# Kernel optimization log

Measured on AMD Instinct MI355X. Metric: run time of the kernel, lower is better.

Reference implementation:

```python
import math
import jax, jax.numpy as jnp
import numpy as np

B, S, D, H = 8, 4096, 1024, 16
DH = D // H


def setup_inputs() -> dict:
    key = jax.random.key(0)
    ks = jax.random.split(key, 12)
    std = 0.02
    inp = {
        "hidden_states": jax.random.normal(ks[0], (B, S, D), jnp.float32),
        "attention_mask": jnp.zeros((B, 1, S), jnp.float32),
        # Linear params stored as (in, out); torch Linear computes x @ W.T + b,
        # equivalent to x @ W_here + b with W_here = W_torch.T
        "Wq": jax.random.normal(ks[1], (D, D), jnp.float32) * std,
        "bq": jnp.zeros((D,), jnp.float32),
        "Wqa": jax.random.normal(ks[2], (D, H), jnp.float32) * std,
        "bqa": jnp.zeros((H,), jnp.float32),
        "Wk": jax.random.normal(ks[3], (D, D), jnp.float32) * std,
        "bk": jnp.zeros((D,), jnp.float32),
        "Wka": jax.random.normal(ks[4], (D, H), jnp.float32) * std,
        "bka": jnp.zeros((H,), jnp.float32),
        "Wt": jax.random.normal(ks[5], (D, D), jnp.float32) * std,
        "bt": jnp.zeros((D,), jnp.float32),
    }
    return inp


def reference(hidden_states, attention_mask, Wq, bq, Wqa, bqa, Wk, bk, Wka, bka, Wt, bt):
    b, s, d = hidden_states.shape
    h = Wqa.shape[1]
    dh = d // h
    scale = 1.0 / math.sqrt(dh)

    q = hidden_states @ Wq + bq                      # (B,S,D)
    k = hidden_states @ Wk + bk                      # (B,S,D)

    # query pooling weights: (B,H,S)
    q_score = jnp.swapaxes((q @ Wqa + bqa) * scale, 1, 2) + attention_mask
    q_weight = jax.nn.softmax(q_score, axis=-1)

    q_heads = q.reshape(b, s, h, dh)                 # (B,S,H,dh)
    # pooled query per head -> flatten to (B,1,D); broadcast replaces repeat
    pooled_q = jnp.einsum('bhs,bshd->bhd', q_weight, q_heads).reshape(b, 1, d)

    mixed_qk = k * pooled_q                          # (B,S,D)

    # key pooling weights: (B,H,S)
    k_score = jnp.swapaxes((mixed_qk @ Wka + bka) * scale, 1, 2) + attention_mask
    k_weight = jax.nn.softmax(k_score, axis=-1)

    k_heads = mixed_qk.reshape(b, s, h, dh)
    pooled_k = jnp.einsum('bhs,bshd->bhd', k_weight, k_heads)   # (B,H,dh)

    weighted = (pooled_k[:, None, :, :] * q_heads).reshape(b, s, d)  # (B,S,D)
    return weighted @ Wt + bt + q
```

## Files before the change

kernel.cpp:

```cpp
#include <hip/hip_runtime.h>


typedef unsigned short u16;
typedef float f32x4 __attribute__((ext_vector_type(4)));
typedef short bf16x8 __attribute__((ext_vector_type(8)));

#define DEV __device__ __forceinline__

DEV u16 f2bf(float f) {
  union { float f; unsigned u; } c; c.f = f;
  return (u16)((c.u + 0x7FFFu + ((c.u >> 16) & 1u)) >> 16);
}
DEV float bf2f(u16 h) {
  union { unsigned u; float f; } c; c.u = ((unsigned)h) << 16;
  return c.f;
}

#define SBAR_ __builtin_amdgcn_s_barrier()

__global__ __launch_bounds__(256) void k_cvt(const float* __restrict__ in,
                                             u16* __restrict__ out, int n4) {
  int i = blockIdx.x * 256 + threadIdx.x;
  const int stride = gridDim.x * 256;
  for (; i < n4; i += stride) {
    float4 v = reinterpret_cast<const float4*>(in)[i];
    ushort4 o;
    o.x = f2bf(v.x); o.y = f2bf(v.y); o.z = f2bf(v.z); o.w = f2bf(v.w);
    reinterpret_cast<ushort4*>(out)[i] = o;
  }
}

__global__ __launch_bounds__(256) void k_transw(const float* __restrict__ Wq,
                                                const float* __restrict__ Wk,
                                                const float* __restrict__ Wt,
                                                u16* __restrict__ Wqkt,
                                                u16* __restrict__ Wtt) {
  __shared__ float tile[32][33];
  const int z = blockIdx.z;
  const float* W = (z == 0) ? Wq : (z == 1) ? Wk : Wt;
  u16* D = (z == 0) ? Wqkt : (z == 1) ? (Wqkt + 1024 * 1024) : Wtt;
  const int bn = blockIdx.x, bk = blockIdx.y;
  const int tx = threadIdx.x & 31, ty = threadIdx.x >> 5;
#pragma unroll
  for (int j = 0; j < 4; ++j)
    tile[ty + j * 8][tx] = W[(size_t)(bk * 32 + ty + j * 8) * 1024 + bn * 32 + tx];
  __syncthreads();
#pragma unroll
  for (int j = 0; j < 4; ++j)
    D[(size_t)(bn * 32 + ty + j * 8) * 1024 + bk * 32 + tx] = f2bf(tile[tx][ty + j * 8]);
}

__global__ __launch_bounds__(256) void k_wbt(const u16* __restrict__ Wtt,
                                             const float* __restrict__ pkr,
                                             const float* __restrict__ pqr,
                                             const float* __restrict__ sumk,
                                             const float* __restrict__ sumq,
                                             u16* __restrict__ Wbt) {
  const int i = blockIdx.x * 256 + threadIdx.x;
  const int k0 = (i & 127) * 8;
  const int n  = (i >> 7) & 1023;
  const int b  = i >> 17;
  const int hh = k0 >> 6;
  const float inv = 1.0f / (sumk[b * 16 + hh] * sumq[b * 16 + hh]);
  bf16x8 wv = *reinterpret_cast<const bf16x8*>(&Wtt[n * 1024 + k0]);
  bf16x8 o;
#pragma unroll
  for (int j = 0; j < 8; ++j) {
    const float p = pkr[b * 1024 + k0 + j] * pqr[b * 1024 + k0 + j] * inv;
    const float ident = (k0 + j == n) ? 1.0f : 0.0f;
    o[j] = (short)f2bf(bf2f((u16)wv[j]) * p + ident);
  }
  *reinterpret_cast<bf16x8*>(&Wbt[(size_t)b * 1048576 + (size_t)n * 1024 + k0]) = o;
}

template <int EPI>
__global__ __launch_bounds__(512, 2) void k_gemm8(const u16* __restrict__ A,
                                                  const u16* __restrict__ Bt,
                                                  const float* __restrict__ bias0,
                                                  const float* __restrict__ bias1,
                                                  float* __restrict__ Cf,
                                                  u16* __restrict__ C0,
                                                  u16* __restrict__ C1,
                                                  int gcols) {
  __shared__ __align__(16) u16 lds[2 * 32768];
  const int tid = threadIdx.x;
  const int w = tid >> 6, lane = tid & 63;
  const int wm = w >> 2, wn = w & 3;

  const int nwg = gridDim.x;
  const int swz = (blockIdx.x & 7) * (nwg >> 3) + (blockIdx.x >> 3);
  const int ci = swz % gcols, ri = swz / gcols;
  const int row0 = ri * 256, col0 = ci * 256;

  const int sr = tid >> 3;
  const int ls8 = ((tid & 7) ^ (sr & 7)) * 8;
  const u16* gA = A + (size_t)(row0 + sr) * 1024 + ls8;
  const u16* gB;
  if (EPI == 2) {
    gB = Bt + (size_t)(row0 >> 12) * 1048576 + (size_t)(col0 + sr) * 1024 + ls8;
  } else {
    gB = Bt + (size_t)(col0 + sr) * 1024 + ls8;
  }

  auto stage = [&](int buf, int mat, int half, int kt, const u16* g) {
#pragma unroll
    for (int p = 0; p < 2; ++p) {
      const u16* src = g + (size_t)(half * 128 + p * 64) * 1024 + kt;
      u16* dst = (u16*)&lds[buf * 32768 + mat * 16384 + half * 8192 + p * 4096 + w * 512];
      __builtin_amdgcn_global_load_lds(
          (const __attribute__((address_space(1))) void*)src,
          (__attribute__((address_space(3))) void*)dst, 16, 0, 0);
    }
  };

  f32x4 acc[8][4] = {};

  stage(0, 0, 0, 0, gA);
  stage(0, 0, 1, 0, gA);
  stage(0, 1, 0, 0, gB);
  stage(0, 1, 1, 0, gB);
  stage(1, 1, 0, 64, gB);
  stage(1, 1, 1, 64, gB);
  asm volatile("s_waitcnt vmcnt(4)" ::: "memory");
  SBAR_;

  const int lr15 = lane & 15, lhi = lane >> 4, lx = lane & 7;
  bf16x8 A0f[4][2], A1f[4][2], B0f[2][2], B1f[2][2];

#define RD_Ah(dst, base, half)                                                 \
  _Pragma("unroll") for (int mi = 0; mi < 4; ++mi)                             \
  _Pragma("unroll") for (int ks = 0; ks < 2; ++ks)                             \
    dst[mi][ks] = *reinterpret_cast<const bf16x8*>(                            \
        &(base)[(wm * 128 + (half) * 64 + mi * 16 + lr15) * 64 +               \
                (((ks << 2) | lhi) ^ lx) * 8]);
#define RD_Bh(dst, base, half)                                                 \
  _Pragma("unroll") for (int ni = 0; ni < 2; ++ni)                             \
  _Pragma("unroll") for (int ks = 0; ks < 2; ++ks)                             \
    dst[ni][ks] = *reinterpret_cast<const bf16x8*>(                            \
        &(base)[(wn * 64 + (half) * 32 + ni * 16 + lr15) * 64 +                \
                (((ks << 2) | lhi) ^ lx) * 8]);
#define MFMA_Q(ar, br, mo, no)                                                 \
  _Pragma("unroll") for (int mi = 0; mi < 4; ++mi)                             \
  _Pragma("unroll") for (int ni = 0; ni < 2; ++ni)                             \
  _Pragma("unroll") for (int ks = 0; ks < 2; ++ks)                             \
    acc[(mo) + mi][(no) + ni] = __builtin_amdgcn_mfma_f32_16x16x32_bf16(       \
        ar[mi][ks], br[ni][ks], acc[(mo) + mi][(no) + ni], 0, 0, 0);

#define LGKM0_ asm volatile("s_waitcnt lgkmcnt(0)" ::: "memory")
#define LGKM8_ asm volatile("s_waitcnt lgkmcnt(8)" ::: "memory")
#define PRIO1_ __builtin_amdgcn_s_setprio(1)
#define PRIO0_ __builtin_amdgcn_s_setprio(0)

  const u16* bA0 = &lds[0];
  const u16* bB0 = bA0 + 16384;
  const u16* bA1 = &lds[32768];
  const u16* bB1 = bA1 + 16384;

  for (int i = 0; i < 8; ++i) {
    const int t1k = (2 * i + 1) * 64;
    const int t2k = (2 * i + 2) * 64;
    const int t3k = (2 * i + 3) * 64;
    const bool pf = (i < 7);

    RD_Ah(A0f, bA0, 0);
    RD_Bh(B0f, bB0, 0);
    stage(1, 0, 0, t1k, gA);
    LGKM8_;
    SBAR_;
    LGKM0_;
    PRIO1_; MFMA_Q(A0f, B0f, 0, 0); PRIO0_;
    SBAR_;

    RD_Bh(B1f, bB0, 1);
    stage(1, 0, 1, t1k, gA);
    SBAR_;
    LGKM0_;
    PRIO1_; MFMA_Q(A0f, B1f, 0, 2); PRIO0_;
    SBAR_;

    RD_Ah(A1f, bA0, 1);
    if (pf) stage(0, 1, 0, t2k, gB);
    SBAR_;
    LGKM0_;
    PRIO1_; MFMA_Q(A1f, B1f, 4, 2); PRIO0_;
    SBAR_;

    if (pf) {
      stage(0, 1, 1, t2k, gB);
      asm volatile("s_waitcnt vmcnt(4)" ::: "memory");
    } else {
      asm volatile("s_waitcnt vmcnt(0)" ::: "memory");
    }
    SBAR_;
    PRIO1_; MFMA_Q(A1f, B0f, 4, 0); PRIO0_;
    SBAR_;

    RD_Ah(A0f, bA1, 0);
    RD_Bh(B0f, bB1, 0);
    if (pf) stage(0, 0, 0, t2k, gA);
    LGKM8_;
    SBAR_;
    LGKM0_;
    PRIO1_; MFMA_Q(A0f, B0f, 0, 0); PRIO0_;
    SBAR_;

    RD_Bh(B1f, bB1, 1);
    if (pf) stage(0, 0, 1, t2k, gA);
    SBAR_;
    LGKM0_;
    PRIO1_; MFMA_Q(A0f, B1f, 0, 2); PRIO0_;
    SBAR_;

    RD_Ah(A1f, bA1, 1);
    if (pf) stage(1, 1, 0, t3k, gB);
    SBAR_;
    LGKM0_;
    PRIO1_; MFMA_Q(A1f, B1f, 4, 2); PRIO0_;
    SBAR_;

    if (pf) {
      stage(1, 1, 1, t3k, gB);
      asm volatile("s_waitcnt vmcnt(4)" ::: "memory");
    }
    SBAR_;
    PRIO1_; MFMA_Q(A1f, B0f, 4, 0); PRIO0_;
    SBAR_;
  }
#undef RD_Ah
#undef RD_Bh
#undef MFMA_Q
#undef LGKM0_
#undef LGKM8_
#undef PRIO1_
#undef PRIO0_

  if constexpr (EPI == 0) {
    u16* cl = (u16*)lds;
    const bool lo = (ci < (gcols >> 1));
    const float* bias = lo ? bias0 : bias1;
    u16* dst = lo ? C0 : C1;
    const int colloc0 = col0 - (lo ? 0 : 1024);
#pragma unroll
    for (int n = 0; n < 4; ++n) {
      const int cc = wn * 64 + n * 16 + lr15;
      const float bv = bias[colloc0 + cc];
#pragma unroll
      for (int m = 0; m < 8; ++m) {
        const int rb = wm * 128 + m * 16 + lhi * 4;
#pragma unroll
        for (int j = 0; j < 4; ++j) {
          const int r = rb + j;
          cl[r * 256 + (cc ^ ((r & 12) << 2))] = f2bf(acc[m][n][j] + bv);
        }
      }
    }
    __syncthreads();
#pragma unroll
    for (int pass = 0; pass < 16; ++pass) {
      const int idx = pass * 512 + tid;
      const int r = idx >> 5, g = idx & 31;
      bf16x8 v = *reinterpret_cast<const bf16x8*>(
          &cl[r * 256 + ((g * 8) ^ ((r & 12) << 2))]);
      *reinterpret_cast<bf16x8*>(
          &dst[(size_t)(row0 + r) * 1024 + colloc0 + g * 8]) = v;
    }
  } else {
    float* clf = (float*)lds;
#pragma unroll
    for (int half = 0; half < 2; ++half) {
      __syncthreads();
      if (wm == half) {
#pragma unroll
        for (int n = 0; n < 4; ++n) {
          const int cc = wn * 64 + n * 16 + lr15;
#pragma unroll
          for (int m = 0; m < 8; ++m) {
            const int rb = m * 16 + lhi * 4;
#pragma unroll
            for (int j = 0; j < 4; ++j) {
              const int r = rb + j;
              clf[r * 256 + (cc ^ ((r & 12) << 2))] = acc[m][n][j];
            }
          }
        }
      }
      __syncthreads();
#pragma unroll
      for (int pass = 0; pass < 16; ++pass) {
        const int idx = pass * 512 + tid;
        const int r = idx >> 6, g = idx & 63;
        f32x4 v = *reinterpret_cast<const f32x4*>(
            &clf[r * 256 + ((g * 4) ^ ((r & 12) << 2))]);
        const int grow = row0 + half * 128 + r;
        const int gcol = col0 + g * 4;
        float4 o;
        o.x = v[0] + bias0[gcol + 0];
        o.y = v[1] + bias0[gcol + 1];
        o.z = v[2] + bias0[gcol + 2];
        o.w = v[3] + bias0[gcol + 3];
        *reinterpret_cast<float4*>(&Cf[(size_t)grow * 1024 + gcol]) = o;
      }
    }
  }
}

template <int HAS_PQ>
__global__ __launch_bounds__(256, 2) void k_scoreg(const u16* __restrict__ X,
                                                   const float* __restrict__ Wa,
                                                   const float* __restrict__ bias,
                                                   const float* __restrict__ mask,
                                                   const float* __restrict__ pqr,
                                                   const float* __restrict__ sumq,
                                                   float* __restrict__ wexp,
                                                   float* __restrict__ sumexp,
                                                   float scale) {
  __shared__ __align__(16) u16 bw[16 * 1024];
  __shared__ __align__(16) u16 lA[2 * 128 * 64];
  __shared__ float invs[16];
  const int tid = threadIdx.x;
  const int w = tid >> 6, lane = tid & 63;
  const int row0 = blockIdx.x * 128;
  const int b = row0 >> 12;
  const int si0 = row0 & 4095;

  if (HAS_PQ) {
    if (tid < 16) invs[tid] = 1.0f / sumq[b * 16 + tid];
    __syncthreads();
  }
  for (int t = tid; t < 16384; t += 256) {
    const int k = t >> 4, h = t & 15;
    float wv = Wa[t];
    if (HAS_PQ) wv *= pqr[b * 1024 + k] * invs[k >> 6];
    bw[h * 1024 + (k ^ ((h & 7) << 3))] = f2bf(wv);
  }

  const int sr = tid >> 3;
  const int ls8 = ((tid & 7) ^ (sr & 7)) * 8;
  const u16* gA = X + (size_t)(row0 + sr) * 1024 + ls8;
  auto stage = [&](int buf, int kt) {
#pragma unroll
    for (int p = 0; p < 4; ++p) {
      const u16* src = gA + (size_t)(p * 32) * 1024 + kt;
      u16* dst = &lA[buf * 8192 + p * 2048 + tid * 8];
      __builtin_amdgcn_global_load_lds(
          (const __attribute__((address_space(1))) void*)src,
          (__attribute__((address_space(3))) void*)dst, 16, 0, 0);
    }
  };

  f32x4 acc[2] = {};
  stage(0, 0);
  stage(1, 64);
  asm volatile("s_waitcnt vmcnt(4) lgkmcnt(0)" ::: "memory");
  SBAR_;

  const int lr15 = lane & 15, lhi = lane >> 4, lx = lane & 7;
  bf16x8 Af[2][2], Bf[2];

  int cur = 0;
  for (int t = 0; t < 16; ++t) {
    const u16* bA = &lA[cur * 8192];
    const int kt = t * 64;
#pragma unroll
    for (int mi = 0; mi < 2; ++mi)
#pragma unroll
      for (int ks = 0; ks < 2; ++ks)
        Af[mi][ks] = *reinterpret_cast<const bf16x8*>(
            &bA[(w * 32 + mi * 16 + lr15) * 64 + (((ks << 2) | lhi) ^ lx) * 8]);
#pragma unroll
    for (int ks = 0; ks < 2; ++ks)
      Bf[ks] = *reinterpret_cast<const bf16x8*>(
          &bw[lr15 * 1024 + ((kt + ks * 32 + lhi * 8) ^ ((lr15 & 7) << 3))]);
#pragma unroll
    for (int mi = 0; mi < 2; ++mi)
#pragma unroll
      for (int ks = 0; ks < 2; ++ks)
        acc[mi] = __builtin_amdgcn_mfma_f32_16x16x32_bf16(
            Af[mi][ks], Bf[ks], acc[mi], 0, 0, 0);
    SBAR_;
    if (t < 14) {
      stage(cur, (t + 2) * 64);
      asm volatile("s_waitcnt vmcnt(4)" ::: "memory");
    } else if (t == 14) {
      asm volatile("s_waitcnt vmcnt(0)" ::: "memory");
    }
    SBAR_;
    cur ^= 1;
  }
  SBAR_;

  float* wl = (float*)lA;
#pragma unroll
  for (int mi = 0; mi < 2; ++mi)
#pragma unroll
    for (int j = 0; j < 4; ++j) {
      const int row = w * 32 + mi * 16 + lhi * 4 + j;
      const float v = (acc[mi][j] + bias[lr15]) * scale +
                      mask[b * 4096 + si0 + row];
      wl[lr15 * 132 + row] = __expf(v);
    }
  __syncthreads();
  {
    const int h = tid >> 4, part = tid & 15;
    float s = 0.f;
#pragma unroll
    for (int j = 0; j < 8; ++j) s += wl[h * 132 + part * 8 + j];
#pragma unroll
    for (int m = 1; m < 16; m <<= 1) s += __shfl_xor(s, m, 64);
    if (part == 0) atomicAdd(&sumexp[b * 16 + h], s);
  }
  if (tid < 128) {
    const int h = tid >> 3, g = tid & 7;
#pragma unroll
    for (int q4 = 0; q4 < 4; ++q4) {
      f32x4 v = *reinterpret_cast<const f32x4*>(&wl[h * 132 + g * 16 + q4 * 4]);
      *reinterpret_cast<f32x4*>(
          &wexp[((size_t)b * 16 + h) * 4096 + si0 + g * 16 + q4 * 4]) = v;
    }
  }
}

__global__ __launch_bounds__(256) void k_pool(const float* __restrict__ wexp,
                                              const u16* __restrict__ X,
                                              float* __restrict__ pooled) {
  __shared__ float wl[16][132];
  const int b = blockIdx.x >> 5, c = blockIdx.x & 31;
  const int s0 = c * 128;
  for (int t = threadIdx.x; t < 2048; t += 256) {
    const int h = t >> 7, si = t & 127;
    wl[h][si] = wexp[((size_t)b * 16 + h) * 4096 + s0 + si];
  }
  __syncthreads();
  const int d0 = threadIdx.x * 4, h = threadIdx.x >> 4;
  float a0 = 0, a1 = 0, a2 = 0, a3 = 0;
#pragma unroll 4
  for (int si = 0; si < 128; ++si) {
    const float wv = wl[h][si];
    const size_t base = ((size_t)b * 4096 + s0 + si) * 1024 + d0;
    ushort4 xq = *reinterpret_cast<const ushort4*>(X + base);
    a0 += wv * bf2f(xq.x); a1 += wv * bf2f(xq.y);
    a2 += wv * bf2f(xq.z); a3 += wv * bf2f(xq.w);
  }
  atomicAdd(&pooled[b * 1024 + d0 + 0], a0);
  atomicAdd(&pooled[b * 1024 + d0 + 1], a1);
  atomicAdd(&pooled[b * 1024 + d0 + 2], a2);
  atomicAdd(&pooled[b * 1024 + d0 + 3], a3);
}

extern "C" void kernel_launch(void* const* d_in, const int* in_sizes, int n_in,
                              void* d_out, int out_size, void* d_ws, size_t ws_size,
                              hipStream_t stream) {
  (void)in_sizes; (void)n_in; (void)out_size; (void)ws_size;
  const float* x    = (const float*)d_in[0];
  const float* mask = (const float*)d_in[1];
  const float* Wq   = (const float*)d_in[2];
  const float* bq   = (const float*)d_in[3];
  const float* Wqa  = (const float*)d_in[4];
  const float* bqa  = (const float*)d_in[5];
  const float* Wk   = (const float*)d_in[6];
  const float* bk   = (const float*)d_in[7];
  const float* Wka  = (const float*)d_in[8];
  const float* bka  = (const float*)d_in[9];
  const float* Wt   = (const float*)d_in[10];
  const float* bt   = (const float*)d_in[11];
  float* out = (float*)d_out;
  char* ws = (char*)d_ws;

  size_t off = 0;
  auto take = [&](size_t b) { char* p = ws + off; off += (b + 255) & ~(size_t)255; return p; };
  u16*   xb    = (u16*)  take(67108864);
  u16*   qb    = (u16*)  take(67108864);
  u16*   kb    = (u16*)  take(67108864);
  u16*   Wqkt  = (u16*)  take(4194304);
  u16*   Wtt   = (u16*)  take(2097152);
  u16*   Wbt   = (u16*)  take(16777216);
  float* wexp  = (float*)take(2097152);
  char*  nb    = take(68608);
  float* pqr  = (float*)nb;
  float* pkr  = (float*)(nb + 32768);
  float* sumq = (float*)(nb + 65536);
  float* sumk = (float*)(nb + 66048);

  k_cvt<<<2048, 256, 0, stream>>>(x, xb, 8388608);
  k_transw<<<dim3(32, 32, 3), 256, 0, stream>>>(Wq, Wk, Wt, Wqkt, Wtt);
  hipMemsetAsync(nb, 0, 68608, stream);

  k_gemm8<0><<<1024, 512, 0, stream>>>(xb, Wqkt, bq, bk, nullptr, qb, kb, 8);

  k_scoreg<0><<<256, 256, 0, stream>>>(qb, Wqa, bqa, mask, nullptr, nullptr,
                                       wexp, sumq, 0.125f);
  k_pool<<<256, 256, 0, stream>>>(wexp, qb, pqr);

  k_scoreg<1><<<256, 256, 0, stream>>>(kb, Wka, bka, mask, pqr, sumq,
                                       wexp, sumk, 0.125f);
  k_pool<<<256, 256, 0, stream>>>(wexp, kb, pkr);

  k_wbt<<<4096, 256, 0, stream>>>(Wtt, pkr, pqr, sumk, sumq, Wbt);
  k_gemm8<2><<<512, 512, 0, stream>>>(qb, Wbt, bt, nullptr, out, nullptr, nullptr, 4);
}
```

Baseline: 362.1 us.

## Fold key projection into pooling algebra to drop the K GEMM

The full K projection GEMM and the bf16 K buffer are removed. The key score weights are folded into combined per-batch matrices, (Wk·diag(pooled_q))·Wka plus bias, so scores come straight from x. Pooled q and pooled k are computed by pooling x per head and then multiplying by the transposed weights in a small kernel. This halves the large first GEMM and cuts intermediate traffic. In exchange it adds a naive weight-combine kernel, 16 MB partial-sum buffers and an extra reduction pass per pooling stage.

```diff
diff --git a/kernel.cpp b/kernel.cpp
--- a/kernel.cpp
+++ b/kernel.cpp
@@ -33,12 +33,13 @@
 __global__ __launch_bounds__(256) void k_transw(const float* __restrict__ Wq,
                                                 const float* __restrict__ Wk,
                                                 const float* __restrict__ Wt,
-                                                u16* __restrict__ Wqkt,
+                                                u16* __restrict__ Wqt,
+                                                u16* __restrict__ Wkt,
                                                 u16* __restrict__ Wtt) {
   __shared__ float tile[32][33];
   const int z = blockIdx.z;
   const float* W = (z == 0) ? Wq : (z == 1) ? Wk : Wt;
-  u16* D = (z == 0) ? Wqkt : (z == 1) ? (Wqkt + 1024 * 1024) : Wtt;
+  u16* D = (z == 0) ? Wqt : (z == 1) ? Wkt : Wtt;
   const int bn = blockIdx.x, bk = blockIdx.y;
   const int tx = threadIdx.x & 31, ty = threadIdx.x >> 5;
 #pragma unroll
@@ -50,23 +51,49 @@
     D[(size_t)(bn * 32 + ty + j * 8) * 1024 + bk * 32 + tx] = f2bf(tile[tx][ty + j * 8]);
 }
 
+template <int WEIGHTED>
+__global__ __launch_bounds__(256) void k_wcmb(const float* __restrict__ Wsrc,
+                                              const float* __restrict__ Wa,
+                                              const float* __restrict__ bsrc,
+                                              const float* __restrict__ ba,
+                                              const float* __restrict__ pqn,
+                                              float* __restrict__ Wc,
+                                              float* __restrict__ bc) {
+  const int b = blockIdx.y;
+  const int e = blockIdx.x * 16 + (threadIdx.x >> 4);
+  const int h = threadIdx.x & 15;
+  float s = 0.f;
+  for (int d = 0; d < 1024; ++d) {
+    float w = Wsrc[(size_t)e * 1024 + d] * Wa[d * 16 + h];
+    if (WEIGHTED) w *= pqn[b * 1024 + d];
+    s += w;
+  }
+  Wc[((size_t)b * 1024 + e) * 16 + h] = s;
+  if (blockIdx.x == 0 && threadIdx.x < 16) {
+    const int hh = threadIdx.x;
+    float sb = ba[hh];
+    for (int d = 0; d < 1024; ++d) {
+      float w = bsrc[d] * Wa[d * 16 + hh];
+      if (WEIGHTED) w *= pqn[b * 1024 + d];
+      sb += w;
+    }
+    bc[b * 16 + hh] = sb;
+  }
+}
+
 __global__ __launch_bounds__(256) void k_wbt(const u16* __restrict__ Wtt,
-                                             const float* __restrict__ pkr,
-                                             const float* __restrict__ pqr,
-                                             const float* __restrict__ sumk,
-                                             const float* __restrict__ sumq,
+                                             const float* __restrict__ pqn,
+                                             const float* __restrict__ pkn,
                                              u16* __restrict__ Wbt) {
   const int i = blockIdx.x * 256 + threadIdx.x;
   const int k0 = (i & 127) * 8;
   const int n  = (i >> 7) & 1023;
   const int b  = i >> 17;
-  const int hh = k0 >> 6;
-  const float inv = 1.0f / (sumk[b * 16 + hh] * sumq[b * 16 + hh]);
   bf16x8 wv = *reinterpret_cast<const bf16x8*>(&Wtt[n * 1024 + k0]);
   bf16x8 o;
 #pragma unroll
   for (int j = 0; j < 8; ++j) {
-    const float p = pkr[b * 1024 + k0 + j] * pqr[b * 1024 + k0 + j] * inv;
+    const float p = pqn[b * 1024 + k0 + j] * pkn[b * 1024 + k0 + j];
     const float ident = (k0 + j == n) ? 1.0f : 0.0f;
     o[j] = (short)f2bf(bf2f((u16)wv[j]) * p + ident);
   }
@@ -77,10 +104,8 @@
 __global__ __launch_bounds__(512, 2) void k_gemm8(const u16* __restrict__ A,
                                                   const u16* __restrict__ Bt,
                                                   const float* __restrict__ bias0,
-                                                  const float* __restrict__ bias1,
                                                   float* __restrict__ Cf,
                                                   u16* __restrict__ C0,
-                                                  u16* __restrict__ C1,
                                                   int gcols) {
   __shared__ __align__(16) u16 lds[2 * 32768];
   const int tid = threadIdx.x;
@@ -236,14 +261,10 @@
 
   if constexpr (EPI == 0) {
     u16* cl = (u16*)lds;
-    const bool lo = (ci < (gcols >> 1));
-    const float* bias = lo ? bias0 : bias1;
-    u16* dst = lo ? C0 : C1;
-    const int colloc0 = col0 - (lo ? 0 : 1024);
 #pragma unroll
     for (int n = 0; n < 4; ++n) {
       const int cc = wn * 64 + n * 16 + lr15;
-      const float bv = bias[colloc0 + cc];
+      const float bv = bias0[col0 + cc];
 #pragma unroll
       for (int m = 0; m < 8; ++m) {
         const int rb = wm * 128 + m * 16 + lhi * 4;
@@ -262,7 +283,7 @@
       bf16x8 v = *reinterpret_cast<const bf16x8*>(
           &cl[r * 256 + ((g * 8) ^ ((r & 12) << 2))]);
       *reinterpret_cast<bf16x8*>(
-          &dst[(size_t)(row0 + r) * 1024 + colloc0 + g * 8]) = v;
+          &C0[(size_t)(row0 + r) * 1024 + col0 + g * 8]) = v;
     }
   } else {
     float* clf = (float*)lds;
@@ -304,34 +325,27 @@
   }
 }
 
-template <int HAS_PQ>
 __global__ __launch_bounds__(256, 2) void k_scoreg(const u16* __restrict__ X,
-                                                   const float* __restrict__ Wa,
+                                                   const float* __restrict__ Weff,
                                                    const float* __restrict__ bias,
                                                    const float* __restrict__ mask,
-                                                   const float* __restrict__ pqr,
-                                                   const float* __restrict__ sumq,
                                                    float* __restrict__ wexp,
                                                    float* __restrict__ sumexp,
-                                                   float scale) {
+                                                   float scale, int wstride,
+                                                   int bstride) {
   __shared__ __align__(16) u16 bw[16 * 1024];
   __shared__ __align__(16) u16 lA[2 * 128 * 64];
-  __shared__ float invs[16];
   const int tid = threadIdx.x;
   const int w = tid >> 6, lane = tid & 63;
   const int row0 = blockIdx.x * 128;
   const int b = row0 >> 12;
   const int si0 = row0 & 4095;
 
-  if (HAS_PQ) {
-    if (tid < 16) invs[tid] = 1.0f / sumq[b * 16 + tid];
-    __syncthreads();
-  }
+  const float* Wb = Weff + (size_t)b * wstride;
+  const float* bb = bias + b * bstride;
   for (int t = tid; t < 16384; t += 256) {
     const int k = t >> 4, h = t & 15;
-    float wv = Wa[t];
-    if (HAS_PQ) wv *= pqr[b * 1024 + k] * invs[k >> 6];
-    bw[h * 1024 + (k ^ ((h & 7) << 3))] = f2bf(wv);
+    bw[h * 1024 + (k ^ ((h & 7) << 3))] = f2bf(Wb[t]);
   }
 
   const int sr = tid >> 3;
@@ -395,7 +409,7 @@
 #pragma unroll
     for (int j = 0; j < 4; ++j) {
       const int row = w * 32 + mi * 16 + lhi * 4 + j;
-      const float v = (acc[mi][j] + bias[lr15]) * scale +
+      const float v = (acc[mi][j] + bb[lr15]) * scale +
                       mask[b * 4096 + si0 + row];
       wl[lr15 * 132 + row] = __expf(v);
     }
@@ -420,9 +434,9 @@
   }
 }
 
-__global__ __launch_bounds__(256) void k_pool(const float* __restrict__ wexp,
-                                              const u16* __restrict__ X,
-                                              float* __restrict__ pooled) {
+__global__ __launch_bounds__(256) void k_poolx(const float* __restrict__ wexp,
+                                               const u16* __restrict__ X,
+                                               float* __restrict__ PXpart) {
   __shared__ float wl[16][132];
   const int b = blockIdx.x >> 5, c = blockIdx.x & 31;
   const int s0 = c * 128;
@@ -431,20 +445,59 @@
     wl[h][si] = wexp[((size_t)b * 16 + h) * 4096 + s0 + si];
   }
   __syncthreads();
-  const int d0 = threadIdx.x * 4, h = threadIdx.x >> 4;
+  const int e0 = threadIdx.x * 4;
+  float acc[16][4] = {};
+#pragma unroll 2
+  for (int si = 0; si < 128; ++si) {
+    const size_t base = ((size_t)b * 4096 + s0 + si) * 1024 + e0;
+    ushort4 xq = *reinterpret_cast<const ushort4*>(X + base);
+    const float x0 = bf2f(xq.x), x1 = bf2f(xq.y), x2 = bf2f(xq.z), x3 = bf2f(xq.w);
+#pragma unroll
+    for (int h = 0; h < 16; ++h) {
+      const float wv = wl[h][si];
+      acc[h][0] += wv * x0; acc[h][1] += wv * x1;
+      acc[h][2] += wv * x2; acc[h][3] += wv * x3;
+    }
+  }
+  float* dst = PXpart + (size_t)(b * 32 + c) * 16384;
+#pragma unroll
+  for (int h = 0; h < 16; ++h) {
+    f32x4 v; v[0] = acc[h][0]; v[1] = acc[h][1]; v[2] = acc[h][2]; v[3] = acc[h][3];
+    *reinterpret_cast<f32x4*>(&dst[h * 1024 + e0]) = v;
+  }
+}
+
+__global__ __launch_bounds__(256) void k_pxw(const float* __restrict__ PXpart,
+                                             const u16* __restrict__ WT,
+                                             const float* __restrict__ bvec,
+                                             const float* __restrict__ sum,
+                                             float* __restrict__ outn) {
+  __shared__ float pxs[1024];
+  const int h = blockIdx.x & 15, b = blockIdx.x >> 4;
+  const int t = threadIdx.x;
   float a0 = 0, a1 = 0, a2 = 0, a3 = 0;
-#pragma unroll 4
-  for (int si = 0; si < 128; ++si) {
-    const float wv = wl[h][si];
-    const size_t base = ((size_t)b * 4096 + s0 + si) * 1024 + d0;
-    ushort4 xq = *reinterpret_cast<const ushort4*>(X + base);
-    a0 += wv * bf2f(xq.x); a1 += wv * bf2f(xq.y);
-    a2 += wv * bf2f(xq.z); a3 += wv * bf2f(xq.w);
-  }
-  atomicAdd(&pooled[b * 1024 + d0 + 0], a0);
-  atomicAdd(&pooled[b * 1024 + d0 + 1], a1);
-  atomicAdd(&pooled[b * 1024 + d0 + 2], a2);
-  atomicAdd(&pooled[b * 1024 + d0 + 3], a3);
+  for (int cc = 0; cc < 32; ++cc) {
+    const float* src = PXpart + (size_t)(b * 32 + cc) * 16384 + h * 1024 + t * 4;
+    f32x4 v = *reinterpret_cast<const f32x4*>(src);
+    a0 += v[0]; a1 += v[1]; a2 += v[2]; a3 += v[3];
+  }
+  pxs[t * 4 + 0] = a0; pxs[t * 4 + 1] = a1;
+  pxs[t * 4 + 2] = a2; pxs[t * 4 + 3] = a3;
+  __syncthreads();
+  const int d = h * 64 + (t >> 2), c4 = t & 3;
+  float p = 0.f;
+  for (int i = 0; i < 32; ++i) {
+    bf16x8 wv = *reinterpret_cast<const bf16x8*>(&WT[(size_t)d * 1024 + c4 * 256 + i * 8]);
+#pragma unroll
+    for (int j = 0; j < 8; ++j)
+      p += pxs[c4 * 256 + i * 8 + j] * bf2f((u16)wv[j]);
+  }
+  p += __shfl_xor(p, 1, 64);
+  p += __shfl_xor(p, 2, 64);
+  if (c4 == 0) {
+    const float sv = sum[b * 16 + h];
+    outn[b * 1024 + d] = (p + bvec[d] * sv) / sv;
+  }
 }
 
 extern "C" void kernel_launch(void* const* d_in, const int* in_sizes, int n_in,
@@ -470,31 +523,39 @@
   auto take = [&](size_t b) { char* p = ws + off; off += (b + 255) & ~(size_t)255; return p; };
   u16*   xb    = (u16*)  take(67108864);
   u16*   qb    = (u16*)  take(67108864);
-  u16*   kb    = (u16*)  take(67108864);
-  u16*   Wqkt  = (u16*)  take(4194304);
+  u16*   Wqt   = (u16*)  take(2097152);
+  u16*   Wkt   = (u16*)  take(2097152);
   u16*   Wtt   = (u16*)  take(2097152);
   u16*   Wbt   = (u16*)  take(16777216);
   float* wexp  = (float*)take(2097152);
-  char*  nb    = take(68608);
-  float* pqr  = (float*)nb;
-  float* pkr  = (float*)(nb + 32768);
-  float* sumq = (float*)(nb + 65536);
-  float* sumk = (float*)(nb + 66048);
+  float* PXp   = (float*)take(16777216);
+  float* Wcq   = (float*)take(65536);
+  float* Wck   = (float*)take(524288);
+  float* pqn   = (float*)take(32768);
+  float* pkn   = (float*)take(32768);
+  char*  nb    = take(2048);
+  float* sumq  = (float*)nb;
+  float* sumk  = (float*)(nb + 512);
+  float* bcq   = (float*)(nb + 1024);
+  float* bck   = (float*)(nb + 1536);
 
   k_cvt<<<2048, 256, 0, stream>>>(x, xb, 8388608);
-  k_transw<<<dim3(32, 32, 3), 256, 0, stream>>>(Wq, Wk, Wt, Wqkt, Wtt);
-  hipMemsetAsync(nb, 0, 68608, stream);
-
-  k_gemm8<0><<<1024, 512, 0, stream>>>(xb, Wqkt, bq, bk, nullptr, qb, kb, 8);
-
-  k_scoreg<0><<<256, 256, 0, stream>>>(qb, Wqa, bqa, mask, nullptr, nullptr,
-                                       wexp, sumq, 0.125f);
-  k_pool<<<256, 256, 0, stream>>>(wexp, qb, pqr);
-
-  k_scoreg<1><<<256, 256, 0, stream>>>(kb, Wka, bka, mask, pqr, sumq,
-                                       wexp, sumk, 0.125f);
-  k_pool<<<256, 256, 0, stream>>>(wexp, kb, pkr);
-
-  k_wbt<<<4096, 256, 0, stream>>>(Wtt, pkr, pqr, sumk, sumq, Wbt);
-  k_gemm8<2><<<512, 512, 0, stream>>>(qb, Wbt, bt, nullptr, out, nullptr, nullptr, 4);
-}
+  k_transw<<<dim3(32, 32, 3), 256, 0, stream>>>(Wq, Wk, Wt, Wqt, Wkt, Wtt);
+  hipMemsetAsync(nb, 0, 2048, stream);
+  k_wcmb<0><<<dim3(64, 1), 256, 0, stream>>>(Wq, Wqa, bq, bqa, nullptr, Wcq, bcq);
+
+  k_gemm8<0><<<512, 512, 0, stream>>>(xb, Wqt, bq, nullptr, qb, 4);
+
+  k_scoreg<<<256, 256, 0, stream>>>(xb, Wcq, bcq, mask, wexp, sumq, 0.125f, 0, 0);
+  k_poolx<<<256, 256, 0, stream>>>(wexp, xb, PXp);
+  k_pxw<<<128, 256, 0, stream>>>(PXp, Wqt, bq, sumq, pqn);
+
+  k_wcmb<1><<<dim3(64, 8), 256, 0, stream>>>(Wk, Wka, bk, bka, pqn, Wck, bck);
+  k_scoreg<<<256, 256, 0, stream>>>(xb, Wck, bck, mask, wexp, sumk, 0.125f,
+                                    16384, 16);
+  k_poolx<<<256, 256, 0, stream>>>(wexp, xb, PXp);
+  k_pxw<<<128, 256, 0, stream>>>(PXp, Wkt, bk, sumk, pkn);
+
+  k_wbt<<<4096, 256, 0, stream>>>(Wtt, pqn, pkn, Wbt);
+  k_gemm8<2><<<512, 512, 0, stream>>>(qb, Wbt, bt, out, nullptr, 4);
+}
```

After: 485.7 us. 1.34x slower.

## Fuse softmax-weighted pooling into the score kernel, dropping separate pool launches

Applied to the files above, without the earlier changes.

The score kernel now keeps its 128 exponentiated weights per head in shared memory and uses them directly to accumulate the pooled query/key vectors over its own 128-row slice, adding partial sums with atomics. This removes the two standalone pool kernels and the intermediate weight buffer they wrote and then read back. The bf16 rows are re-read right after the score tile loaded them, so they are more likely to come from cache. The cost is a longer per-block tail in the score kernel and possibly higher register pressure.

```diff
diff --git a/kernel.cpp b/kernel.cpp
--- a/kernel.cpp
+++ b/kernel.cpp
@@ -311,7 +311,7 @@
                                                    const float* __restrict__ mask,
                                                    const float* __restrict__ pqr,
                                                    const float* __restrict__ sumq,
-                                                   float* __restrict__ wexp,
+                                                   float* __restrict__ pooled,
                                                    float* __restrict__ sumexp,
                                                    float scale) {
   __shared__ __align__(16) u16 bw[16 * 1024];
@@ -409,42 +409,22 @@
     for (int m = 1; m < 16; m <<= 1) s += __shfl_xor(s, m, 64);
     if (part == 0) atomicAdd(&sumexp[b * 16 + h], s);
   }
-  if (tid < 128) {
-    const int h = tid >> 3, g = tid & 7;
-#pragma unroll
-    for (int q4 = 0; q4 < 4; ++q4) {
-      f32x4 v = *reinterpret_cast<const f32x4*>(&wl[h * 132 + g * 16 + q4 * 4]);
-      *reinterpret_cast<f32x4*>(
-          &wexp[((size_t)b * 16 + h) * 4096 + si0 + g * 16 + q4 * 4]) = v;
-    }
-  }
-}
-
-__global__ __launch_bounds__(256) void k_pool(const float* __restrict__ wexp,
-                                              const u16* __restrict__ X,
-                                              float* __restrict__ pooled) {
-  __shared__ float wl[16][132];
-  const int b = blockIdx.x >> 5, c = blockIdx.x & 31;
-  const int s0 = c * 128;
-  for (int t = threadIdx.x; t < 2048; t += 256) {
-    const int h = t >> 7, si = t & 127;
-    wl[h][si] = wexp[((size_t)b * 16 + h) * 4096 + s0 + si];
-  }
-  __syncthreads();
-  const int d0 = threadIdx.x * 4, h = threadIdx.x >> 4;
-  float a0 = 0, a1 = 0, a2 = 0, a3 = 0;
+  {
+    const int d0 = tid * 4, hh = tid >> 4;
+    float a0 = 0, a1 = 0, a2 = 0, a3 = 0;
 #pragma unroll 4
-  for (int si = 0; si < 128; ++si) {
-    const float wv = wl[h][si];
-    const size_t base = ((size_t)b * 4096 + s0 + si) * 1024 + d0;
-    ushort4 xq = *reinterpret_cast<const ushort4*>(X + base);
-    a0 += wv * bf2f(xq.x); a1 += wv * bf2f(xq.y);
-    a2 += wv * bf2f(xq.z); a3 += wv * bf2f(xq.w);
-  }
-  atomicAdd(&pooled[b * 1024 + d0 + 0], a0);
-  atomicAdd(&pooled[b * 1024 + d0 + 1], a1);
-  atomicAdd(&pooled[b * 1024 + d0 + 2], a2);
-  atomicAdd(&pooled[b * 1024 + d0 + 3], a3);
+    for (int si = 0; si < 128; ++si) {
+      const float wv = wl[hh * 132 + si];
+      const size_t base = (size_t)(row0 + si) * 1024 + d0;
+      ushort4 xq = *reinterpret_cast<const ushort4*>(X + base);
+      a0 += wv * bf2f(xq.x); a1 += wv * bf2f(xq.y);
+      a2 += wv * bf2f(xq.z); a3 += wv * bf2f(xq.w);
+    }
+    atomicAdd(&pooled[b * 1024 + d0 + 0], a0);
+    atomicAdd(&pooled[b * 1024 + d0 + 1], a1);
+    atomicAdd(&pooled[b * 1024 + d0 + 2], a2);
+    atomicAdd(&pooled[b * 1024 + d0 + 3], a3);
+  }
 }
 
 extern "C" void kernel_launch(void* const* d_in, const int* in_sizes, int n_in,
@@ -474,7 +454,6 @@
   u16*   Wqkt  = (u16*)  take(4194304);
   u16*   Wtt   = (u16*)  take(2097152);
   u16*   Wbt   = (u16*)  take(16777216);
-  float* wexp  = (float*)take(2097152);
   char*  nb    = take(68608);
   float* pqr  = (float*)nb;
   float* pkr  = (float*)(nb + 32768);
@@ -488,12 +467,10 @@
   k_gemm8<0><<<1024, 512, 0, stream>>>(xb, Wqkt, bq, bk, nullptr, qb, kb, 8);
 
   k_scoreg<0><<<256, 256, 0, stream>>>(qb, Wqa, bqa, mask, nullptr, nullptr,
-                                       wexp, sumq, 0.125f);
-  k_pool<<<256, 256, 0, stream>>>(wexp, qb, pqr);
+                                       pqr, sumq, 0.125f);
 
   k_scoreg<1><<<256, 256, 0, stream>>>(kb, Wka, bka, mask, pqr, sumq,
-                                       wexp, sumk, 0.125f);
-  k_pool<<<256, 256, 0, stream>>>(wexp, kb, pkr);
+                                       pkr, sumk, 0.125f);
 
   k_wbt<<<4096, 256, 0, stream>>>(Wtt, pkr, pqr, sumk, sumq, Wbt);
   k_gemm8<2><<<512, 512, 0, stream>>>(qb, Wbt, bt, nullptr, out, nullptr, nullptr, 4);
```

After: 354.4 us. 2.1% less time.
